# Optimization experiments

Hardware: AMD Instinct MI355X
Metric: run time of the kernel (lower is better)

## Reference

```python
import jax, jax.numpy as jnp
import numpy as np

MODES_X = 16
MODES_Y = 16


def setup_inputs() -> dict:
    key = jax.random.key(0)
    ks = jax.random.split(key, 8)
    B, H, W, C = 32, 128, 128, 64
    scale = 1.0 / (C * C)
    x = jax.random.normal(ks[0], (B, H, W, C), dtype=jnp.float32)
    w1_real = scale * jax.random.normal(ks[1], (MODES_X, MODES_Y, C, C), dtype=jnp.float32)
    w1_imag = scale * jax.random.normal(ks[2], (MODES_X, MODES_Y, C, C), dtype=jnp.float32)
    w2_real = scale * jax.random.normal(ks[3], (MODES_X, MODES_Y, C, C), dtype=jnp.float32)
    w2_imag = scale * jax.random.normal(ks[4], (MODES_X, MODES_Y, C, C), dtype=jnp.float32)
    dense_kernel = jax.random.normal(ks[5], (C, C), dtype=jnp.float32) / np.sqrt(C)
    dense_bias = jnp.zeros((C,), dtype=jnp.float32)
    return {"x": x, "w1_real": w1_real, "w1_imag": w1_imag,
            "w2_real": w2_real, "w2_imag": w2_imag,
            "dense_kernel": dense_kernel, "dense_bias": dense_bias}


def _spectral_conv2d(x, w1, w2, mx, my):
    # x: [B,H,W,C] real; w1,w2: [mx,my,C,C] complex
    B, H, W, C = x.shape
    x_ft = jnp.fft.rfft2(x, axes=(1, 2))  # [B,H,W//2+1,C] complex64
    out_ft = jnp.zeros((B, H, W // 2 + 1, C), dtype=x_ft.dtype)
    # low positive x-frequencies
    out_ft = out_ft.at[:, :mx, :my].set(
        jnp.einsum('bxyi,xyio->bxyo', x_ft[:, :mx, :my], w1))
    # low negative x-frequencies
    out_ft = out_ft.at[:, -mx:, :my].set(
        jnp.einsum('bxyi,xyio->bxyo', x_ft[:, -mx:, :my], w2))
    return jnp.fft.irfft2(out_ft, s=(H, W), axes=(1, 2))


def reference(x, w1_real, w1_imag, w2_real, w2_imag, dense_kernel, dense_bias):
    w1 = w1_real + 1j * w1_imag
    w2 = w2_real + 1j * w2_imag
    y_s = _spectral_conv2d(x, w1, w2, MODES_X, MODES_Y)
    y_p = jnp.einsum('bhwi,io->bhwo', x, dense_kernel) + dense_bias
    return jax.nn.gelu(x + y_s + y_p, approximate=True)
```

## Files before the change

### kernel.cpp

```cpp
#include <hip/hip_runtime.h>
#include <math.h>

#define BB 32
#define HH 128
#define WW 128
#define CC 64
#define MX 16
#define MY 16
#define NKX 32

#define TWOPI 6.283185307179586f

typedef __attribute__((ext_vector_type(8))) short bf16x8;
typedef __attribute__((ext_vector_type(4))) float f32x4;

__device__ inline unsigned short f2bf(float f) {
    union { float f; unsigned u; } v; v.f = f;
    unsigned r = v.u + 0x7FFFu + ((v.u >> 16) & 1u);
    return (unsigned short)(r >> 16);
}



__global__ __launch_bounds__(256) void kA(const float* __restrict__ x, unsigned short* __restrict__ X1) {
    __shared__ float2 tw[128];
    __shared__ short Af[2 * 4 * 64 * 8];
    int tid = threadIdx.x;
    int bh = blockIdx.x;
    if (tid < 128) {
        float s, c;
        sincosf(TWOPI * (float)tid * (1.0f / 128.0f), &s, &c);
        tw[tid] = make_float2(c, s);
    }
    __syncthreads();
    #pragma unroll
    for (int s = 0; s < 2; ++s) {
        int slot = tid + s * 256;
        int l = slot & 63, ks = (slot >> 6) & 3, mt = slot >> 8;
        int q = l >> 4, r = l & 15;
        int row = mt * 16 + r;
        int ky = row >> 1, ri = row & 1;
        int k0 = ks * 32 + q * 8;
        short v[8];
        #pragma unroll
        for (int e = 0; e < 8; ++e) {
            float2 t = tw[(ky * (k0 + e)) & 127];
            v[e] = (short)f2bf(ri ? -t.y : t.x);
        }
        *(bf16x8*)&Af[slot * 8] = *(const bf16x8*)v;
    }
    __syncthreads();

    int lane = tid & 63, wid = tid >> 6;
    int q = lane >> 4, r = lane & 15;
    int nt = wid;
    const float* xp = x + (size_t)bh * (WW * CC);
    bf16x8 bf[4];
    #pragma unroll
    for (int ks = 0; ks < 4; ++ks) {
        short v[8];
        #pragma unroll
        for (int e = 0; e < 8; ++e)
            v[e] = (short)f2bf(xp[(ks * 32 + q * 8 + e) * CC + nt * 16 + r]);
        bf[ks] = *(const bf16x8*)v;
    }
    f32x4 acc0 = {0.f, 0.f, 0.f, 0.f}, acc1 = {0.f, 0.f, 0.f, 0.f};
    #pragma unroll
    for (int ks = 0; ks < 4; ++ks) {
        bf16x8 a0 = *(const bf16x8*)&Af[((0 * 4 + ks) * 64 + lane) * 8];
        bf16x8 a1 = *(const bf16x8*)&Af[((1 * 4 + ks) * 64 + lane) * 8];
        acc0 = __builtin_amdgcn_mfma_f32_16x16x32_bf16(a0, bf[ks], acc0, 0, 0, 0);
        acc1 = __builtin_amdgcn_mfma_f32_16x16x32_bf16(a1, bf[ks], acc1, 0, 0, 0);
    }
    int b = bh >> 7, h = bh & 127;
    int c = nt * 16 + r;
    #pragma unroll
    for (int j = 0; j < 4; ++j) {
        int m0 = q * 4 + j;
        X1[(((size_t)b * 16 + (m0 >> 1)) * 128 + h) * 128 + (m0 & 1) * 64 + c] = f2bf(acc0[j]);
        int m1 = 16 + m0;
        X1[(((size_t)b * 16 + (m1 >> 1)) * 128 + h) * 128 + (m1 & 1) * 64 + c] = f2bf(acc1[j]);
    }
}

__global__ __launch_bounds__(256) void kB(const unsigned short* __restrict__ X1, unsigned short* __restrict__ X2) {
    __shared__ float2 tw[128];
    __shared__ short Af[4 * 8 * 64 * 8];
    int tid = threadIdx.x;
    if (tid < 128) {
        float s, c;
        sincosf(TWOPI * (float)tid * (1.0f / 128.0f), &s, &c);
        tw[tid] = make_float2(c, s);
    }
    __syncthreads();
    #pragma unroll
    for (int s = 0; s < 8; ++s) {
        int slot = tid + s * 256;
        int l = slot & 63, ks = (slot >> 6) & 7, mt = slot >> 9;
        int q = l >> 4, r = l & 15;
        int row = mt * 16 + r;
        int kxi = row >> 1, rr = row & 1;
        int kx = (kxi < 16) ? kxi : (96 + kxi);
        int k0 = ks * 32 + q * 8;
        short v[8];
        #pragma unroll
        for (int e = 0; e < 8; ++e) {
            int k = k0 + e;
            int h = k >> 1, ri = k & 1;
            float2 t = tw[(kx * h) & 127];
            float val = (rr == 0) ? (ri == 0 ? t.x : t.y) : (ri == 0 ? -t.y : t.x);
            v[e] = (short)f2bf(val);
        }
        *(bf16x8*)&Af[slot * 8] = *(const bf16x8*)v;
    }
    __syncthreads();

    int blk = blockIdx.x;
    int b = blk >> 4, ky = blk & 15;
    const unsigned short* p = X1 + ((size_t)b * 16 + ky) * 16384;
    int lane = tid & 63, wid = tid >> 6;
    int q = lane >> 4, r = lane & 15;
    int col = wid * 16 + r;
    bf16x8 bf[8];
    #pragma unroll
    for (int ks = 0; ks < 8; ++ks) {
        short v[8];
        #pragma unroll
        for (int e = 0; e < 8; ++e)
            v[e] = (short)p[(ks * 32 + q * 8 + e) * 64 + col];
        bf[ks] = *(const bf16x8*)v;
    }
    f32x4 acc[4] = {{0.f,0.f,0.f,0.f},{0.f,0.f,0.f,0.f},{0.f,0.f,0.f,0.f},{0.f,0.f,0.f,0.f}};
    #pragma unroll
    for (int ks = 0; ks < 8; ++ks) {
        #pragma unroll
        for (int mt = 0; mt < 4; ++mt) {
            bf16x8 a = *(const bf16x8*)&Af[((mt * 8 + ks) * 64 + lane) * 8];
            acc[mt] = __builtin_amdgcn_mfma_f32_16x16x32_bf16(a, bf[ks], acc[mt], 0, 0, 0);
        }
    }
    #pragma unroll
    for (int mt = 0; mt < 4; ++mt) {
        #pragma unroll
        for (int j = 0; j < 4; ++j) {
            int m = mt * 16 + q * 4 + j;
            int kxi = m >> 1, rr = m & 1;
            X2[(((size_t)b * NKX + kxi) * 16 + ky) * 128 + 2 * col + rr] = f2bf(acc[mt][j]);
        }
    }
}

__global__ __launch_bounds__(256) void kC(const float* __restrict__ w1r, const float* __restrict__ w1i,
                                          const float* __restrict__ w2r, const float* __restrict__ w2i,
                                          const unsigned short* __restrict__ X2, unsigned short* __restrict__ G) {
    __shared__ float wsr[CC * CC];
    __shared__ float wsi[CC * CC];
    int tid = threadIdx.x;
    int blk = blockIdx.x;
    int kxi = blk >> 4, ky = blk & 15;
    const float* wr = (kxi < 16) ? w1r : w2r;
    const float* wi = (kxi < 16) ? w1i : w2i;
    int wx = (kxi < 16) ? kxi : (kxi - 16);
    size_t woff = ((size_t)wx * MY + ky) * (CC * CC);
    for (int i = tid * 4; i < CC * CC; i += 1024) {
        *(float4*)&wsr[i] = *(const float4*)&wr[woff + i];
        *(float4*)&wsi[i] = *(const float4*)&wi[woff + i];
    }
    __syncthreads();

    int lane = tid & 63, wid = tid >> 6;
    int q = lane >> 4, r = lane & 15;
    bf16x8 af[2][4];
    #pragma unroll
    for (int mt = 0; mt < 2; ++mt) {
        int b = mt * 16 + r;
        #pragma unroll
        for (int ks = 0; ks < 4; ++ks)
            af[mt][ks] = *(const bf16x8*)&X2[(((size_t)b * NKX + kxi) * 16 + ky) * 128 + ks * 32 + q * 8];
    }
    bf16x8 bfr[2][4];
    #pragma unroll
    for (int t = 0; t < 2; ++t) {
        int n = (wid * 2 + t) * 16 + r;
        int o = n >> 1, ro = n & 1;
        #pragma unroll
        for (int ks = 0; ks < 4; ++ks) {
            short v[8];
            #pragma unroll
            for (int e = 0; e < 8; ++e) {
                int k = ks * 32 + q * 8 + e;
                int i = k >> 1, ri = k & 1;
                float val = (ri == 0) ? (ro ? wsi[i * 64 + o] : wsr[i * 64 + o])
                                      : (ro ? wsr[i * 64 + o] : -wsi[i * 64 + o]);
                v[e] = (short)f2bf(val);
            }
            bfr[t][ks] = *(const bf16x8*)v;
        }
    }
    f32x4 acc[2][2] = {{{0.f,0.f,0.f,0.f},{0.f,0.f,0.f,0.f}},{{0.f,0.f,0.f,0.f},{0.f,0.f,0.f,0.f}}};
    #pragma unroll
    for (int ks = 0; ks < 4; ++ks)
        #pragma unroll
        for (int mt = 0; mt < 2; ++mt)
            #pragma unroll
            for (int t = 0; t < 2; ++t)
                acc[mt][t] = __builtin_amdgcn_mfma_f32_16x16x32_bf16(af[mt][ks], bfr[t][ks], acc[mt][t], 0, 0, 0);
    #pragma unroll
    for (int mt = 0; mt < 2; ++mt)
        #pragma unroll
        for (int t = 0; t < 2; ++t)
            #pragma unroll
            for (int j = 0; j < 4; ++j) {
                int b = mt * 16 + q * 4 + j;
                int n = (wid * 2 + t) * 16 + r;
                G[(((size_t)b * NKX + kxi) * 16 + ky) * 128 + n] = f2bf(acc[mt][t][j]);
            }
}

__global__ __launch_bounds__(256) void kD(const unsigned short* __restrict__ G, unsigned short* __restrict__ Z) {
    __shared__ float2 tw[128];
    __shared__ short Af[8 * 2 * 64 * 8];
    int tid = threadIdx.x;
    if (tid < 128) {
        float s, c;
        sincosf(TWOPI * (float)tid * (1.0f / 128.0f), &s, &c);
        tw[tid] = make_float2(c, s);
    }
    __syncthreads();
    #pragma unroll
    for (int s = 0; s < 4; ++s) {
        int slot = tid + s * 256;
        int l = slot & 63, ks = (slot >> 6) & 1, mt = slot >> 7;
        int q = l >> 4, r = l & 15;
        int h = mt * 16 + r;
        int k0 = ks * 32 + q * 8;
        short v[8];
        #pragma unroll
        for (int e = 0; e < 8; ++e) {
            int k = k0 + e;
            int kxi = k >> 1, ri = k & 1;
            int kx = (kxi < 16) ? kxi : (96 + kxi);
            float2 t = tw[(kx * h) & 127];
            v[e] = (short)f2bf(ri == 0 ? t.x : -t.y);
        }
        *(bf16x8*)&Af[slot * 8] = *(const bf16x8*)v;
    }
    __syncthreads();

    int blk = blockIdx.x;
    int b = blk >> 4, ky = blk & 15;
    int lane = tid & 63, wid = tid >> 6;
    int q = lane >> 4, r = lane & 15;
    bf16x8 bfr[2][2];
    #pragma unroll
    for (int t = 0; t < 2; ++t) {
        int n = (wid * 2 + t) * 16 + r;
        #pragma unroll
        for (int ks = 0; ks < 2; ++ks) {
            short v[8];
            #pragma unroll
            for (int e = 0; e < 8; ++e) {
                int k = ks * 32 + q * 8 + e;
                int kxi = k >> 1, ri = k & 1;
                unsigned short raw = G[(((size_t)b * NKX + kxi) * 16 + ky) * 128 + (n ^ ri)];
                if (ri & (n & 1)) raw ^= 0x8000u;
                v[e] = (short)raw;
            }
            bfr[t][ks] = *(const bf16x8*)v;
        }
    }
    f32x4 acc[8][2];
    #pragma unroll
    for (int mt = 0; mt < 8; ++mt)
        #pragma unroll
        for (int t = 0; t < 2; ++t)
            acc[mt][t] = (f32x4){0.f, 0.f, 0.f, 0.f};
    #pragma unroll
    for (int ks = 0; ks < 2; ++ks)
        #pragma unroll
        for (int mt = 0; mt < 8; ++mt) {
            bf16x8 a = *(const bf16x8*)&Af[((mt * 2 + ks) * 64 + lane) * 8];
            #pragma unroll
            for (int t = 0; t < 2; ++t)
                acc[mt][t] = __builtin_amdgcn_mfma_f32_16x16x32_bf16(a, bfr[t][ks], acc[mt][t], 0, 0, 0);
        }
    #pragma unroll
    for (int mt = 0; mt < 8; ++mt)
        #pragma unroll
        for (int t = 0; t < 2; ++t)
            #pragma unroll
            for (int j = 0; j < 4; ++j) {
                int h = mt * 16 + q * 4 + j;
                int n = (wid * 2 + t) * 16 + r;
                Z[(((size_t)b * HH + h) * 16 + ky) * 128 + n] = f2bf(acc[mt][t][j]);
            }
}

__global__ __launch_bounds__(256, 2) void kE(const float* __restrict__ x, const unsigned short* __restrict__ Zb,
                                             const float* __restrict__ K, const float* __restrict__ bias,
                                             float* __restrict__ out) {
    __shared__ float xs[WW * CC];
    __shared__ short Afrag[8 * 3 * 64 * 8];
    __shared__ short Bfrag[4 * 3 * 64 * 8];
    __shared__ float2 tw[128];
    int tid = threadIdx.x;
    int bh = blockIdx.x;
    if (tid < 128) {
        float s, c;
        sincosf(TWOPI * (float)tid * (1.0f / 128.0f), &s, &c);
        tw[tid] = make_float2(c, s);
    }
    const float* xp = x + (size_t)bh * (WW * CC);
    for (int i = tid * 4; i < WW * CC; i += 1024)
        *(float4*)&xs[i] = *(const float4*)&xp[i];
    __syncthreads();

    const float inv = 1.0f / 16384.0f;
    #pragma unroll
    for (int s = 0; s < 6; ++s) {
        int slot = tid + s * 256;
        int l = slot & 63;
        int ks = (slot >> 6) % 3;
        int tm = slot / 192;
        int q = l >> 4, r = l & 15;
        int row = tm * 16 + r;
        short v[8];
        if (ks < 2) {
            int k0 = ks * 32 + q * 8;
            #pragma unroll
            for (int e = 0; e < 8; ++e) v[e] = (short)f2bf(xs[row * CC + k0 + e]);
        } else {
            #pragma unroll
            for (int e = 0; e < 8; ++e) {
                int ky = 4 * q + (e >> 1);
                float sc = ((ky == 0) ? 1.0f : 2.0f) * inv;
                float2 t = tw[(ky * row) & 127];
                float val = (e & 1) ? (-t.y * sc) : (t.x * sc);
                v[e] = (short)f2bf(val);
            }
        }
        *(bf16x8*)&Afrag[slot * 8] = *(const bf16x8*)v;
    }
    #pragma unroll
    for (int s = 0; s < 3; ++s) {
        int slot = tid + s * 256;
        int l = slot & 63;
        int ks = (slot >> 6) % 3;
        int nt = slot / 192;
        int q = l >> 4, r = l & 15;
        int col = nt * 16 + r;
        short v[8];
        if (ks < 2) {
            #pragma unroll
            for (int e = 0; e < 8; ++e) {
                int k = ks * 32 + q * 8 + e;
                v[e] = (short)f2bf(K[k * CC + col]);
            }
        } else {
            #pragma unroll
            for (int e = 0; e < 8; ++e) {
                int kp = q * 8 + e;
                v[e] = (short)Zb[(size_t)bh * 2048 + (kp >> 1) * 128 + 2 * col + (kp & 1)];
            }
        }
        *(bf16x8*)&Bfrag[slot * 8] = *(const bf16x8*)v;
    }
    __syncthreads();

    int lane = tid & 63;
    int wv = tid >> 6;
    int q = lane >> 4, r = lane & 15;
    #pragma unroll
    for (int nt = 0; nt < 4; ++nt) {
        #pragma unroll
        for (int t2 = 0; t2 < 2; ++t2) {
            int tm = wv * 2 + t2;
            f32x4 acc = {0.f, 0.f, 0.f, 0.f};
            #pragma unroll
            for (int ks = 0; ks < 3; ++ks) {
                bf16x8 a = *(const bf16x8*)&Afrag[((tm * 3 + ks) * 64 + lane) * 8];
                bf16x8 b = *(const bf16x8*)&Bfrag[((nt * 3 + ks) * 64 + lane) * 8];
                acc = __builtin_amdgcn_mfma_f32_16x16x32_bf16(a, b, acc, 0, 0, 0);
            }
            int c = nt * 16 + r;
            float bsv = bias[c];
            #pragma unroll
            for (int j = 0; j < 4; ++j) {
                int w = tm * 16 + q * 4 + j;
                float u = acc[j] + xs[w * CC + c] + bsv;
                float t = u + 0.044715f * u * u * u;
                float e = __expf(-1.5957691216057308f * t);
                out[(size_t)bh * (WW * CC) + w * CC + c] = u / (1.0f + e);
            }
        }
    }
}

extern "C" void kernel_launch(void* const* d_in, const int* in_sizes, int n_in,
                              void* d_out, int out_size, void* d_ws, size_t ws_size,
                              hipStream_t stream) {
    const float* x   = (const float*)d_in[0];
    const float* w1r = (const float*)d_in[1];
    const float* w1i = (const float*)d_in[2];
    const float* w2r = (const float*)d_in[3];
    const float* w2i = (const float*)d_in[4];
    const float* dk  = (const float*)d_in[5];
    const float* db  = (const float*)d_in[6];
    float* out = (float*)d_out;

    unsigned short* X1 = (unsigned short*)d_ws;
    unsigned short* X2 = X1 + 8388608;
    unsigned short* G  = X2 + 2097152;
    unsigned short* Z  = G  + 2097152;

    kA<<<BB * HH, 256, 0, stream>>>(x, X1);
    kB<<<BB * MY, 256, 0, stream>>>(X1, X2);
    kC<<<NKX * MY, 256, 0, stream>>>(w1r, w1i, w2r, w2i, X2, G);
    kD<<<BB * MY, 256, 0, stream>>>(G, Z);
    kE<<<BB * HH, 256, 0, stream>>>(x, Z, dk, db, out);
}
```

Measured before the change: 319.4 us.

## Precompute DFT twiddle and dense-weight MFMA fragments once in a setup kernel

Adds a small kernel kT that builds every bf16 DFT twiddle fragment and the dense-kernel fragment once into workspace. kA, kB, kD and kE now read these fragments from global memory instead of running sincos and fragment assembly in shared memory in every block. kD is split into two blocks per (b,ky) and writes Z directly in the MFMA fragment layout that kE consumes. kE pads its x tile in shared memory to 68 floats per row to reduce bank conflicts. The trade is an extra launch plus per-block global/L2 fragment loads, in place of redundant per-block trig and shared-memory setup and two barriers per block.

```diff
diff --git a/kernel.cpp b/kernel.cpp
--- a/kernel.cpp
+++ b/kernel.cpp
@@ -21,39 +21,86 @@
 }
 
 
-
-__global__ __launch_bounds__(256) void kA(const float* __restrict__ x, unsigned short* __restrict__ X1) {
+__global__ __launch_bounds__(256) void kT(const float* __restrict__ K, unsigned short* __restrict__ FR) {
     __shared__ float2 tw[128];
-    __shared__ short Af[2 * 4 * 64 * 8];
     int tid = threadIdx.x;
-    int bh = blockIdx.x;
     if (tid < 128) {
         float s, c;
         sincosf(TWOPI * (float)tid * (1.0f / 128.0f), &s, &c);
         tw[tid] = make_float2(c, s);
     }
     __syncthreads();
-    #pragma unroll
-    for (int s = 0; s < 2; ++s) {
-        int slot = tid + s * 256;
-        int l = slot & 63, ks = (slot >> 6) & 3, mt = slot >> 8;
-        int q = l >> 4, r = l & 15;
-        int row = mt * 16 + r;
-        int ky = row >> 1, ri = row & 1;
+    int g = blockIdx.x * 256 + tid;
+    short v[8];
+    if (g < 512) {
+        int s = g;
+        int l = s & 63, ks = (s >> 6) & 3, mt = s >> 8;
+        int q = l >> 4, r = l & 15;
+        int row = mt * 16 + r, ky = row >> 1, ri = row & 1;
         int k0 = ks * 32 + q * 8;
-        short v[8];
         #pragma unroll
         for (int e = 0; e < 8; ++e) {
             float2 t = tw[(ky * (k0 + e)) & 127];
             v[e] = (short)f2bf(ri ? -t.y : t.x);
         }
-        *(bf16x8*)&Af[slot * 8] = *(const bf16x8*)v;
-    }
-    __syncthreads();
-
-    int lane = tid & 63, wid = tid >> 6;
-    int q = lane >> 4, r = lane & 15;
-    int nt = wid;
+    } else if (g < 2560) {
+        int s = g - 512;
+        int l = s & 63, ks = (s >> 6) & 7, mt = s >> 9;
+        int q = l >> 4, r = l & 15;
+        int row = mt * 16 + r, kxi = row >> 1, rr = row & 1;
+        int kx = (kxi < 16) ? kxi : (96 + kxi);
+        int k0 = ks * 32 + q * 8;
+        #pragma unroll
+        for (int e = 0; e < 8; ++e) {
+            int k = k0 + e, h = k >> 1, ri = k & 1;
+            float2 t = tw[(kx * h) & 127];
+            float val = (rr == 0) ? (ri == 0 ? t.x : t.y) : (ri == 0 ? -t.y : t.x);
+            v[e] = (short)f2bf(val);
+        }
+    } else if (g < 3584) {
+        int s = g - 2560;
+        int l = s & 63, ks = (s >> 6) & 1, mt = s >> 7;
+        int q = l >> 4, r = l & 15;
+        int h = mt * 16 + r;
+        int k0 = ks * 32 + q * 8;
+        #pragma unroll
+        for (int e = 0; e < 8; ++e) {
+            int k = k0 + e, kxi = k >> 1, ri = k & 1;
+            int kx = (kxi < 16) ? kxi : (96 + kxi);
+            float2 t = tw[(kx * h) & 127];
+            v[e] = (short)f2bf(ri == 0 ? t.x : -t.y);
+        }
+    } else if (g < 4096) {
+        int s = g - 3584;
+        int l = s & 63, tm = s >> 6;
+        int q = l >> 4, r = l & 15;
+        int row = tm * 16 + r;
+        const float inv = 1.0f / 16384.0f;
+        #pragma unroll
+        for (int e = 0; e < 8; ++e) {
+            int ky = 4 * q + (e >> 1);
+            float sc = ((ky == 0) ? 1.0f : 2.0f) * inv;
+            float2 t = tw[(ky * row) & 127];
+            v[e] = (short)f2bf((e & 1) ? (-t.y * sc) : (t.x * sc));
+        }
+    } else {
+        int s = g - 4096;
+        int l = s & 63, ks = (s >> 6) & 1, nt = s >> 7;
+        int q = l >> 4, r = l & 15;
+        int col = nt * 16 + r;
+        #pragma unroll
+        for (int e = 0; e < 8; ++e) {
+            int k = ks * 32 + q * 8 + e;
+            v[e] = (short)f2bf(K[k * CC + col]);
+        }
+    }
+    *(bf16x8*)&FR[(size_t)g * 8] = *(const bf16x8*)v;
+}
+
+__global__ __launch_bounds__(256) void kA(const float* __restrict__ x, const unsigned short* __restrict__ FR,
+                                          unsigned short* __restrict__ X1) {
+    int tid = threadIdx.x, bh = blockIdx.x;
+    int lane = tid & 63, nt = tid >> 6, q = lane >> 4, r = lane & 15;
     const float* xp = x + (size_t)bh * (WW * CC);
     bf16x8 bf[4];
     #pragma unroll
@@ -67,8 +114,8 @@
     f32x4 acc0 = {0.f, 0.f, 0.f, 0.f}, acc1 = {0.f, 0.f, 0.f, 0.f};
     #pragma unroll
     for (int ks = 0; ks < 4; ++ks) {
-        bf16x8 a0 = *(const bf16x8*)&Af[((0 * 4 + ks) * 64 + lane) * 8];
-        bf16x8 a1 = *(const bf16x8*)&Af[((1 * 4 + ks) * 64 + lane) * 8];
+        bf16x8 a0 = *(const bf16x8*)&FR[((size_t)((0 * 4 + ks) * 64 + lane)) * 8];
+        bf16x8 a1 = *(const bf16x8*)&FR[((size_t)((1 * 4 + ks) * 64 + lane)) * 8];
         acc0 = __builtin_amdgcn_mfma_f32_16x16x32_bf16(a0, bf[ks], acc0, 0, 0, 0);
         acc1 = __builtin_amdgcn_mfma_f32_16x16x32_bf16(a1, bf[ks], acc1, 0, 0, 0);
     }
@@ -83,43 +130,13 @@
     }
 }
 
-__global__ __launch_bounds__(256) void kB(const unsigned short* __restrict__ X1, unsigned short* __restrict__ X2) {
-    __shared__ float2 tw[128];
-    __shared__ short Af[4 * 8 * 64 * 8];
-    int tid = threadIdx.x;
-    if (tid < 128) {
-        float s, c;
-        sincosf(TWOPI * (float)tid * (1.0f / 128.0f), &s, &c);
-        tw[tid] = make_float2(c, s);
-    }
-    __syncthreads();
-    #pragma unroll
-    for (int s = 0; s < 8; ++s) {
-        int slot = tid + s * 256;
-        int l = slot & 63, ks = (slot >> 6) & 7, mt = slot >> 9;
-        int q = l >> 4, r = l & 15;
-        int row = mt * 16 + r;
-        int kxi = row >> 1, rr = row & 1;
-        int kx = (kxi < 16) ? kxi : (96 + kxi);
-        int k0 = ks * 32 + q * 8;
-        short v[8];
-        #pragma unroll
-        for (int e = 0; e < 8; ++e) {
-            int k = k0 + e;
-            int h = k >> 1, ri = k & 1;
-            float2 t = tw[(kx * h) & 127];
-            float val = (rr == 0) ? (ri == 0 ? t.x : t.y) : (ri == 0 ? -t.y : t.x);
-            v[e] = (short)f2bf(val);
-        }
-        *(bf16x8*)&Af[slot * 8] = *(const bf16x8*)v;
-    }
-    __syncthreads();
-
-    int blk = blockIdx.x;
+__global__ __launch_bounds__(256) void kB(const unsigned short* __restrict__ X1, const unsigned short* __restrict__ FR,
+                                          unsigned short* __restrict__ X2) {
+    int tid = threadIdx.x, blk = blockIdx.x;
     int b = blk >> 4, ky = blk & 15;
+    const unsigned short* FB = FR + 4096;
     const unsigned short* p = X1 + ((size_t)b * 16 + ky) * 16384;
-    int lane = tid & 63, wid = tid >> 6;
-    int q = lane >> 4, r = lane & 15;
+    int lane = tid & 63, wid = tid >> 6, q = lane >> 4, r = lane & 15;
     int col = wid * 16 + r;
     bf16x8 bf[8];
     #pragma unroll
@@ -130,22 +147,19 @@
             v[e] = (short)p[(ks * 32 + q * 8 + e) * 64 + col];
         bf[ks] = *(const bf16x8*)v;
     }
-    f32x4 acc[4] = {{0.f,0.f,0.f,0.f},{0.f,0.f,0.f,0.f},{0.f,0.f,0.f,0.f},{0.f,0.f,0.f,0.f}};
-    #pragma unroll
-    for (int ks = 0; ks < 8; ++ks) {
-        #pragma unroll
-        for (int mt = 0; mt < 4; ++mt) {
-            bf16x8 a = *(const bf16x8*)&Af[((mt * 8 + ks) * 64 + lane) * 8];
-            acc[mt] = __builtin_amdgcn_mfma_f32_16x16x32_bf16(a, bf[ks], acc[mt], 0, 0, 0);
-        }
-    }
     #pragma unroll
     for (int mt = 0; mt < 4; ++mt) {
+        f32x4 acc = {0.f, 0.f, 0.f, 0.f};
+        #pragma unroll
+        for (int ks = 0; ks < 8; ++ks) {
+            bf16x8 a = *(const bf16x8*)&FB[((size_t)((mt * 8 + ks) * 64 + lane)) * 8];
+            acc = __builtin_amdgcn_mfma_f32_16x16x32_bf16(a, bf[ks], acc, 0, 0, 0);
+        }
         #pragma unroll
         for (int j = 0; j < 4; ++j) {
             int m = mt * 16 + q * 4 + j;
             int kxi = m >> 1, rr = m & 1;
-            X2[(((size_t)b * NKX + kxi) * 16 + ky) * 128 + 2 * col + rr] = f2bf(acc[mt][j]);
+            X2[(((size_t)b * NKX + kxi) * 16 + ky) * 128 + 2 * col + rr] = f2bf(acc[j]);
         }
     }
 }
@@ -217,40 +231,12 @@
             }
 }
 
-__global__ __launch_bounds__(256) void kD(const unsigned short* __restrict__ G, unsigned short* __restrict__ Z) {
-    __shared__ float2 tw[128];
-    __shared__ short Af[8 * 2 * 64 * 8];
-    int tid = threadIdx.x;
-    if (tid < 128) {
-        float s, c;
-        sincosf(TWOPI * (float)tid * (1.0f / 128.0f), &s, &c);
-        tw[tid] = make_float2(c, s);
-    }
-    __syncthreads();
-    #pragma unroll
-    for (int s = 0; s < 4; ++s) {
-        int slot = tid + s * 256;
-        int l = slot & 63, ks = (slot >> 6) & 1, mt = slot >> 7;
-        int q = l >> 4, r = l & 15;
-        int h = mt * 16 + r;
-        int k0 = ks * 32 + q * 8;
-        short v[8];
-        #pragma unroll
-        for (int e = 0; e < 8; ++e) {
-            int k = k0 + e;
-            int kxi = k >> 1, ri = k & 1;
-            int kx = (kxi < 16) ? kxi : (96 + kxi);
-            float2 t = tw[(kx * h) & 127];
-            v[e] = (short)f2bf(ri == 0 ? t.x : -t.y);
-        }
-        *(bf16x8*)&Af[slot * 8] = *(const bf16x8*)v;
-    }
-    __syncthreads();
-
-    int blk = blockIdx.x;
-    int b = blk >> 4, ky = blk & 15;
-    int lane = tid & 63, wid = tid >> 6;
-    int q = lane >> 4, r = lane & 15;
+__global__ __launch_bounds__(256) void kD(const unsigned short* __restrict__ G, const unsigned short* __restrict__ FR,
+                                          unsigned short* __restrict__ Zf) {
+    int tid = threadIdx.x, blk = blockIdx.x;
+    int b = blk >> 5, ky = (blk >> 1) & 15, mh = blk & 1;
+    int lane = tid & 63, wid = tid >> 6, q = lane >> 4, r = lane & 15;
+    const unsigned short* FD = FR + 20480;
     bf16x8 bfr[2][2];
     #pragma unroll
     for (int t = 0; t < 2; ++t) {
@@ -269,125 +255,78 @@
             bfr[t][ks] = *(const bf16x8*)v;
         }
     }
-    f32x4 acc[8][2];
-    #pragma unroll
-    for (int mt = 0; mt < 8; ++mt)
-        #pragma unroll
-        for (int t = 0; t < 2; ++t)
-            acc[mt][t] = (f32x4){0.f, 0.f, 0.f, 0.f};
-    #pragma unroll
-    for (int ks = 0; ks < 2; ++ks)
-        #pragma unroll
-        for (int mt = 0; mt < 8; ++mt) {
-            bf16x8 a = *(const bf16x8*)&Af[((mt * 2 + ks) * 64 + lane) * 8];
+    #pragma unroll
+    for (int mt2 = 0; mt2 < 4; ++mt2) {
+        int mt = mh * 4 + mt2;
+        f32x4 acc[2] = {{0.f,0.f,0.f,0.f},{0.f,0.f,0.f,0.f}};
+        #pragma unroll
+        for (int ks = 0; ks < 2; ++ks) {
+            bf16x8 a = *(const bf16x8*)&FD[((size_t)((mt * 2 + ks) * 64 + lane)) * 8];
             #pragma unroll
             for (int t = 0; t < 2; ++t)
-                acc[mt][t] = __builtin_amdgcn_mfma_f32_16x16x32_bf16(a, bfr[t][ks], acc[mt][t], 0, 0, 0);
-        }
-    #pragma unroll
-    for (int mt = 0; mt < 8; ++mt)
+                acc[t] = __builtin_amdgcn_mfma_f32_16x16x32_bf16(a, bfr[t][ks], acc[t], 0, 0, 0);
+        }
         #pragma unroll
         for (int t = 0; t < 2; ++t)
             #pragma unroll
             for (int j = 0; j < 4; ++j) {
                 int h = mt * 16 + q * 4 + j;
                 int n = (wid * 2 + t) * 16 + r;
-                Z[(((size_t)b * HH + h) * 16 + ky) * 128 + n] = f2bf(acc[mt][t][j]);
-            }
-}
-
-__global__ __launch_bounds__(256, 2) void kE(const float* __restrict__ x, const unsigned short* __restrict__ Zb,
-                                             const float* __restrict__ K, const float* __restrict__ bias,
-                                             float* __restrict__ out) {
-    __shared__ float xs[WW * CC];
-    __shared__ short Afrag[8 * 3 * 64 * 8];
-    __shared__ short Bfrag[4 * 3 * 64 * 8];
-    __shared__ float2 tw[128];
-    int tid = threadIdx.x;
-    int bh = blockIdx.x;
-    if (tid < 128) {
-        float s, c;
-        sincosf(TWOPI * (float)tid * (1.0f / 128.0f), &s, &c);
-        tw[tid] = make_float2(c, s);
-    }
+                int c = n >> 1, reim = n & 1;
+                int kp = 2 * ky + reim, q2 = kp >> 3, e2 = kp & 7;
+                int nt2 = c >> 4, r2 = c & 15;
+                Zf[(((size_t)b * 128 + h) * 4 + nt2) * 512 + (q2 * 16 + r2) * 8 + e2] = f2bf(acc[t][j]);
+            }
+    }
+}
+
+__global__ __launch_bounds__(256) void kE(const float* __restrict__ x, const unsigned short* __restrict__ Zf,
+                                          const unsigned short* __restrict__ FR,
+                                          const float* __restrict__ bias, float* __restrict__ out) {
+    __shared__ float xs[WW * 68];
+    int tid = threadIdx.x, bh = blockIdx.x;
     const float* xp = x + (size_t)bh * (WW * CC);
-    for (int i = tid * 4; i < WW * CC; i += 1024)
-        *(float4*)&xs[i] = *(const float4*)&xp[i];
+    for (int i = tid * 4; i < WW * CC; i += 1024) {
+        int w = i >> 6, c = i & 63;
+        *(float4*)&xs[w * 68 + c] = *(const float4*)&xp[i];
+    }
     __syncthreads();
-
-    const float inv = 1.0f / 16384.0f;
-    #pragma unroll
-    for (int s = 0; s < 6; ++s) {
-        int slot = tid + s * 256;
-        int l = slot & 63;
-        int ks = (slot >> 6) % 3;
-        int tm = slot / 192;
-        int q = l >> 4, r = l & 15;
+    int lane = tid & 63, wv = tid >> 6, q = lane >> 4, r = lane & 15;
+    const unsigned short* FEAT = FR + 28672;
+    const unsigned short* FEBK = FR + 32768;
+    bf16x8 ax[2][2], at[2];
+    #pragma unroll
+    for (int t2 = 0; t2 < 2; ++t2) {
+        int tm = wv * 2 + t2;
         int row = tm * 16 + r;
-        short v[8];
-        if (ks < 2) {
-            int k0 = ks * 32 + q * 8;
-            #pragma unroll
-            for (int e = 0; e < 8; ++e) v[e] = (short)f2bf(xs[row * CC + k0 + e]);
-        } else {
-            #pragma unroll
-            for (int e = 0; e < 8; ++e) {
-                int ky = 4 * q + (e >> 1);
-                float sc = ((ky == 0) ? 1.0f : 2.0f) * inv;
-                float2 t = tw[(ky * row) & 127];
-                float val = (e & 1) ? (-t.y * sc) : (t.x * sc);
-                v[e] = (short)f2bf(val);
-            }
-        }
-        *(bf16x8*)&Afrag[slot * 8] = *(const bf16x8*)v;
-    }
-    #pragma unroll
-    for (int s = 0; s < 3; ++s) {
-        int slot = tid + s * 256;
-        int l = slot & 63;
-        int ks = (slot >> 6) % 3;
-        int nt = slot / 192;
-        int q = l >> 4, r = l & 15;
-        int col = nt * 16 + r;
-        short v[8];
-        if (ks < 2) {
-            #pragma unroll
-            for (int e = 0; e < 8; ++e) {
-                int k = ks * 32 + q * 8 + e;
-                v[e] = (short)f2bf(K[k * CC + col]);
-            }
-        } else {
-            #pragma unroll
-            for (int e = 0; e < 8; ++e) {
-                int kp = q * 8 + e;
-                v[e] = (short)Zb[(size_t)bh * 2048 + (kp >> 1) * 128 + 2 * col + (kp & 1)];
-            }
-        }
-        *(bf16x8*)&Bfrag[slot * 8] = *(const bf16x8*)v;
-    }
-    __syncthreads();
-
-    int lane = tid & 63;
-    int wv = tid >> 6;
-    int q = lane >> 4, r = lane & 15;
+        #pragma unroll
+        for (int ks = 0; ks < 2; ++ks) {
+            const float* s = &xs[row * 68 + ks * 32 + q * 8];
+            short v[8];
+            #pragma unroll
+            for (int e = 0; e < 8; ++e) v[e] = (short)f2bf(s[e]);
+            ax[t2][ks] = *(const bf16x8*)v;
+        }
+        at[t2] = *(const bf16x8*)&FEAT[((size_t)(tm * 64 + lane)) * 8];
+    }
     #pragma unroll
     for (int nt = 0; nt < 4; ++nt) {
+        bf16x8 b0 = *(const bf16x8*)&FEBK[((size_t)((nt * 2 + 0) * 64 + lane)) * 8];
+        bf16x8 b1 = *(const bf16x8*)&FEBK[((size_t)((nt * 2 + 1) * 64 + lane)) * 8];
+        bf16x8 bz = *(const bf16x8*)&Zf[((size_t)bh * 4 + nt) * 512 + lane * 8];
+        int c = nt * 16 + r;
+        float bsv = bias[c];
         #pragma unroll
         for (int t2 = 0; t2 < 2; ++t2) {
             int tm = wv * 2 + t2;
             f32x4 acc = {0.f, 0.f, 0.f, 0.f};
-            #pragma unroll
-            for (int ks = 0; ks < 3; ++ks) {
-                bf16x8 a = *(const bf16x8*)&Afrag[((tm * 3 + ks) * 64 + lane) * 8];
-                bf16x8 b = *(const bf16x8*)&Bfrag[((nt * 3 + ks) * 64 + lane) * 8];
-                acc = __builtin_amdgcn_mfma_f32_16x16x32_bf16(a, b, acc, 0, 0, 0);
-            }
-            int c = nt * 16 + r;
-            float bsv = bias[c];
+            acc = __builtin_amdgcn_mfma_f32_16x16x32_bf16(ax[t2][0], b0, acc, 0, 0, 0);
+            acc = __builtin_amdgcn_mfma_f32_16x16x32_bf16(ax[t2][1], b1, acc, 0, 0, 0);
+            acc = __builtin_amdgcn_mfma_f32_16x16x32_bf16(at[t2], bz, acc, 0, 0, 0);
             #pragma unroll
             for (int j = 0; j < 4; ++j) {
                 int w = tm * 16 + q * 4 + j;
-                float u = acc[j] + xs[w * CC + c] + bsv;
+                float u = acc[j] + xs[w * 68 + c] + bsv;
                 float t = u + 0.044715f * u * u * u;
                 float e = __expf(-1.5957691216057308f * t);
                 out[(size_t)bh * (WW * CC) + w * CC + c] = u / (1.0f + e);
@@ -408,14 +347,16 @@
     const float* db  = (const float*)d_in[6];
     float* out = (float*)d_out;
 
-    unsigned short* X1 = (unsigned short*)d_ws;
+    unsigned short* FR = (unsigned short*)d_ws;
+    unsigned short* X1 = FR + 65536;
     unsigned short* X2 = X1 + 8388608;
     unsigned short* G  = X2 + 2097152;
-    unsigned short* Z  = G  + 2097152;
-
-    kA<<<BB * HH, 256, 0, stream>>>(x, X1);
-    kB<<<BB * MY, 256, 0, stream>>>(X1, X2);
+    unsigned short* Zf = G  + 2097152;
+
+    kT<<<18, 256, 0, stream>>>(dk, FR);
+    kA<<<BB * HH, 256, 0, stream>>>(x, FR, X1);
+    kB<<<BB * MY, 256, 0, stream>>>(X1, FR, X2);
     kC<<<NKX * MY, 256, 0, stream>>>(w1r, w1i, w2r, w2i, X2, G);
-    kD<<<BB * MY, 256, 0, stream>>>(G, Z);
-    kE<<<BB * HH, 256, 0, stream>>>(x, Z, dk, db, out);
-}
+    kD<<<BB * MY * 2, 256, 0, stream>>>(G, FR, Zf);
+    kE<<<BB * HH, 256, 0, stream>>>(x, Zf, FR, db, out);
+}
```

After: 321.2 us. Within noise of the previous version (+0.6%).
